# Optimization experiments

Measured on AMD Instinct MI355X. Metric: run time of the kernel, lower is better.

## Reference

```python
import jax, jax.numpy as jnp
import numpy as np

N = 1_000_000
DATA_DIM = 16
N_COND = 8            # conditions 1..8; condition 0 uses the base model (id 0)
N_BUCKETS = 8         # uniform time intervals per condition on [0,1)
N_MODELS = N_COND * N_BUCKETS + 1   # 65, matches num_models+1 in the torch ctor
HIDDEN = 6            # SimpleModel(data_dim, hidden=6, time_embed_dim=6)
IN_DIM = DATA_DIM + 1 # MLP input is cat([data, t], dim=1)


def setup_inputs() -> dict:
    key = jax.random.key(0)
    k_data, k_cond, k_t, k_w1, k_b1, k_w2, k_b2 = jax.random.split(key, 7)
    data = jax.random.normal(k_data, (N, DATA_DIM), dtype=jnp.float32)
    cond = jax.random.randint(k_cond, (N, 1), 0, N_COND + 1).astype(jnp.float32)  # 0..8
    t = jax.random.uniform(k_t, (N, 1), dtype=jnp.float32)                        # [0,1)
    x = jnp.concatenate([data, cond, t], axis=1)  # [N, DATA_DIM+2]
    s1 = 1.0 / np.sqrt(IN_DIM)
    s2 = 1.0 / np.sqrt(HIDDEN)
    W1 = jax.random.uniform(k_w1, (N_MODELS, IN_DIM, HIDDEN), jnp.float32, -s1, s1)
    b1 = jax.random.uniform(k_b1, (N_MODELS, HIDDEN), jnp.float32, -s1, s1)
    W2 = jax.random.uniform(k_w2, (N_MODELS, HIDDEN, DATA_DIM), jnp.float32, -s2, s2)
    b2 = jax.random.uniform(k_b2, (N_MODELS, DATA_DIM), jnp.float32, -s2, s2)
    return {"x": x, "W1": W1, "b1": b1, "W2": W2, "b2": b2}


def _route(cond_f, t):
    # Bucket routing: cond 0 -> model 0 on [0,1); cond c>=1 -> models 1 + (c-1)*8 + floor(t*8).
    # Equivalent to the torch per-(c, [t1,t2)) masked dispatch with uniform breakpoints.
    c = cond_f.astype(jnp.int32)
    bucket = jnp.clip(jnp.floor(t * N_BUCKETS).astype(jnp.int32), 0, N_BUCKETS - 1)
    return jnp.where(c == 0, 0, 1 + (c - 1) * N_BUCKETS + bucket)


def reference(x, W1, b1, W2, b2):
    data = x[:, :-2]
    cond = x[:, -2]
    t = x[:, -1]
    mid = _route(cond, t)                                   # [N] expert id per row
    xin = jnp.concatenate([data, t[:, None]], axis=1)       # [N, IN_DIM]
    # Fused gather-MLP: gather each row's tiny expert weights and apply the 2-layer MLP.
    h = jax.nn.relu(jnp.einsum('ni,nih->nh', xin, W1[mid]) + b1[mid])   # [N, HIDDEN]
    out = jnp.einsum('nh,nhd->nd', h, W2[mid]) + b2[mid]                # [N, DATA_DIM]
    return out
```

## Files before the change

kernel.cpp:

```cpp
#include <hip/hip_runtime.h>


#define NMODELS 65
#define WPM 220
#define NCHUNK 55
#define BLOCK 512

__global__ __launch_bounds__(BLOCK, 4) void mvf_kernel(
    const float* __restrict__ x,
    const float* __restrict__ W1,
    const float* __restrict__ b1,
    const float* __restrict__ W2,
    const float* __restrict__ b2,
    float* __restrict__ out,
    int npts)
{
    __shared__ float4 wlds[NCHUNK][NMODELS];
    const int tid = threadIdx.x;

    float* wf = (float*)wlds;
    for (int e = tid; e < NMODELS * WPM; e += BLOCK) {
        const int m = e / WPM, k = e % WPM;
        float v;
        if (k < 102)      v = W1[m * 102 + k];
        else if (k < 108) v = b1[m * 6 + (k - 102)];
        else if (k < 204) v = W2[m * 96 + (k - 108)];
        else              v = b2[m * 16 + (k - 204)];
        wf[(k >> 2) * (NMODELS * 4) + m * 4 + (k & 3)] = v;
    }
    __syncthreads();

    const int q = blockIdx.x * BLOCK + tid;
    const int p0 = 2 * q;
    if (p0 >= npts) return;

    float xf[36];
    {
        const float4* xr4 = (const float4*)(x + (long)p0 * 18);
        #pragma unroll
        for (int i = 0; i < 9; ++i) {
            float4 v = xr4[i];
            xf[4 * i + 0] = v.x;
            xf[4 * i + 1] = v.y;
            xf[4 * i + 2] = v.z;
            xf[4 * i + 3] = v.w;
        }
    }
    #define XF(pt, i) xf[(pt) * 18 + (i)]

    int mid[2];
    float tt[2];
    #pragma unroll
    for (int pt = 0; pt < 2; ++pt) {
        const float t = XF(pt, 17);
        const int c = (int)XF(pt, 16);
        int bucket = (int)floorf(t * 8.0f);
        bucket = bucket < 0 ? 0 : (bucket > 7 ? 7 : bucket);
        mid[pt] = (c == 0) ? 0 : 1 + (c - 1) * 8 + bucket;
        tt[pt] = t;
    }

    #define CH(cc, pt) wlds[cc][mid[pt]]

    float h[2][6];
    #pragma unroll
    for (int pt = 0; pt < 2; ++pt) {
        float4 c24 = CH(24, pt);
        float4 c25 = CH(25, pt);
        float4 c26 = CH(26, pt);
        const float t = tt[pt];
        h[pt][0] = fmaf(t, c24.x, c25.z);
        h[pt][1] = fmaf(t, c24.y, c25.w);
        h[pt][2] = fmaf(t, c24.z, c26.x);
        h[pt][3] = fmaf(t, c24.w, c26.y);
        h[pt][4] = fmaf(t, c25.x, c26.z);
        h[pt][5] = fmaf(t, c25.y, c26.w);
    }
    #pragma unroll
    for (int r = 0; r < 8; ++r) {
        #pragma unroll
        for (int pt = 0; pt < 2; ++pt) {
            float4 a = CH(3 * r + 0, pt);
            float4 b = CH(3 * r + 1, pt);
            float4 d = CH(3 * r + 2, pt);
            const float x0 = XF(pt, 2 * r), x1 = XF(pt, 2 * r + 1);
            h[pt][0] = fmaf(x0, a.x, h[pt][0]);
            h[pt][1] = fmaf(x0, a.y, h[pt][1]);
            h[pt][2] = fmaf(x0, a.z, h[pt][2]);
            h[pt][3] = fmaf(x0, a.w, h[pt][3]);
            h[pt][4] = fmaf(x0, b.x, h[pt][4]);
            h[pt][5] = fmaf(x0, b.y, h[pt][5]);
            h[pt][0] = fmaf(x1, b.z, h[pt][0]);
            h[pt][1] = fmaf(x1, b.w, h[pt][1]);
            h[pt][2] = fmaf(x1, d.x, h[pt][2]);
            h[pt][3] = fmaf(x1, d.y, h[pt][3]);
            h[pt][4] = fmaf(x1, d.z, h[pt][4]);
            h[pt][5] = fmaf(x1, d.w, h[pt][5]);
        }
    }
    #pragma unroll
    for (int pt = 0; pt < 2; ++pt)
        #pragma unroll
        for (int j = 0; j < 6; ++j)
            h[pt][j] = h[pt][j] > 0.0f ? h[pt][j] : 0.0f;

    #pragma unroll
    for (int half = 0; half < 2; ++half) {
        #pragma unroll
        for (int pt = 0; pt < 2; ++pt) {
            float o[8];
            {
                float4 ba = CH(51 + 2 * half, pt);
                float4 bb = CH(52 + 2 * half, pt);
                o[0] = ba.x; o[1] = ba.y; o[2] = ba.z; o[3] = ba.w;
                o[4] = bb.x; o[5] = bb.y; o[6] = bb.z; o[7] = bb.w;
            }
            #pragma unroll
            for (int j = 0; j < 6; ++j) {
                float4 A = CH(27 + 4 * j + 2 * half + 0, pt);
                float4 B = CH(27 + 4 * j + 2 * half + 1, pt);
                const float hj = h[pt][j];
                o[0] = fmaf(hj, A.x, o[0]);
                o[1] = fmaf(hj, A.y, o[1]);
                o[2] = fmaf(hj, A.z, o[2]);
                o[3] = fmaf(hj, A.w, o[3]);
                o[4] = fmaf(hj, B.x, o[4]);
                o[5] = fmaf(hj, B.y, o[5]);
                o[6] = fmaf(hj, B.z, o[6]);
                o[7] = fmaf(hj, B.w, o[7]);
            }
            float4* orow = (float4*)(out + (long)(p0 + pt) * 16 + half * 8);
            orow[0] = make_float4(o[0], o[1], o[2], o[3]);
            orow[1] = make_float4(o[4], o[5], o[6], o[7]);
        }
    }
    #undef CH
    #undef XF
}

extern "C" void kernel_launch(void* const* d_in, const int* in_sizes, int n_in,
                              void* d_out, int out_size, void* d_ws, size_t ws_size,
                              hipStream_t stream) {
    const float* x  = (const float*)d_in[0];
    const float* W1 = (const float*)d_in[1];
    const float* b1 = (const float*)d_in[2];
    const float* W2 = (const float*)d_in[3];
    const float* b2 = (const float*)d_in[4];
    float* out = (float*)d_out;

    const int npts = in_sizes[0] / 18;
    const int npairs = (npts + 1) / 2;
    const int grid = (npairs + BLOCK - 1) / BLOCK;
    mvf_kernel<<<grid, BLOCK, 0, stream>>>(x, W1, b1, W2, b2, out, npts);
}
```

Baseline: 48.90 us.

## Double block size, load routing fields first, and compute all outputs before storing

Raises the block size to 1024 so the per-block LDS weight staging is amortized over twice as many points. It loads the cond/t float4s first so routing can start while the remaining input loads are in flight. The second layer now keeps all 16 outputs of both points in registers and writes them with consecutive float4 stores at the end. This raises register pressure, which under launch_bounds(1024,4) may cause spills, and the larger block reduces how many blocks can be resident at once.

```diff
diff --git a/kernel.cpp b/kernel.cpp
--- a/kernel.cpp
+++ b/kernel.cpp
@@ -4,7 +4,7 @@
 #define NMODELS 65
 #define WPM 220
 #define NCHUNK 55
-#define BLOCK 512
+#define BLOCK 1024
 
 __global__ __launch_bounds__(BLOCK, 4) void mvf_kernel(
     const float* __restrict__ x,
@@ -34,32 +34,40 @@
     const int p0 = 2 * q;
     if (p0 >= npts) return;
 
+    const float4* xr4 = (const float4*)(x + (long)p0 * 18);
+
     float xf[36];
     {
-        const float4* xr4 = (const float4*)(x + (long)p0 * 18);
-        #pragma unroll
-        for (int i = 0; i < 9; ++i) {
-            float4 v = xr4[i];
-            xf[4 * i + 0] = v.x;
-            xf[4 * i + 1] = v.y;
-            xf[4 * i + 2] = v.z;
-            xf[4 * i + 3] = v.w;
-        }
+        float4 v4 = xr4[4];
+        float4 v8 = xr4[8];
+        xf[16] = v4.x; xf[17] = v4.y; xf[18] = v4.z; xf[19] = v4.w;
+        xf[32] = v8.x; xf[33] = v8.y; xf[34] = v8.z; xf[35] = v8.w;
     }
-    #define XF(pt, i) xf[(pt) * 18 + (i)]
-
     int mid[2];
     float tt[2];
     #pragma unroll
     for (int pt = 0; pt < 2; ++pt) {
-        const float t = XF(pt, 17);
-        const int c = (int)XF(pt, 16);
+        const float t = xf[pt * 18 + 17];
+        const int c = (int)xf[pt * 18 + 16];
         int bucket = (int)floorf(t * 8.0f);
         bucket = bucket < 0 ? 0 : (bucket > 7 ? 7 : bucket);
         mid[pt] = (c == 0) ? 0 : 1 + (c - 1) * 8 + bucket;
         tt[pt] = t;
     }
 
+    #pragma unroll
+    for (int i = 0; i < 4; ++i) {
+        float4 v = xr4[i];
+        xf[4 * i + 0] = v.x; xf[4 * i + 1] = v.y;
+        xf[4 * i + 2] = v.z; xf[4 * i + 3] = v.w;
+    }
+    #pragma unroll
+    for (int i = 5; i < 8; ++i) {
+        float4 v = xr4[i];
+        xf[4 * i + 0] = v.x; xf[4 * i + 1] = v.y;
+        xf[4 * i + 2] = v.z; xf[4 * i + 3] = v.w;
+    }
+    #define XF(pt, i) xf[(pt) * 18 + (i)]
     #define CH(cc, pt) wlds[cc][mid[pt]]
 
     float h[2][6];
@@ -104,38 +112,43 @@
         for (int j = 0; j < 6; ++j)
             h[pt][j] = h[pt][j] > 0.0f ? h[pt][j] : 0.0f;
 
+    float o[2][16];
     #pragma unroll
-    for (int half = 0; half < 2; ++half) {
+    for (int pt = 0; pt < 2; ++pt) {
+        #pragma unroll
+        for (int g = 0; g < 4; ++g) {
+            float4 v = CH(51 + g, pt);
+            o[pt][4 * g + 0] = v.x;
+            o[pt][4 * g + 1] = v.y;
+            o[pt][4 * g + 2] = v.z;
+            o[pt][4 * g + 3] = v.w;
+        }
+    }
+    #pragma unroll
+    for (int j = 0; j < 6; ++j) {
         #pragma unroll
         for (int pt = 0; pt < 2; ++pt) {
-            float o[8];
-            {
-                float4 ba = CH(51 + 2 * half, pt);
-                float4 bb = CH(52 + 2 * half, pt);
-                o[0] = ba.x; o[1] = ba.y; o[2] = ba.z; o[3] = ba.w;
-                o[4] = bb.x; o[5] = bb.y; o[6] = bb.z; o[7] = bb.w;
+            const float hj = h[pt][j];
+            #pragma unroll
+            for (int g = 0; g < 4; ++g) {
+                float4 v = CH(27 + 4 * j + g, pt);
+                o[pt][4 * g + 0] = fmaf(hj, v.x, o[pt][4 * g + 0]);
+                o[pt][4 * g + 1] = fmaf(hj, v.y, o[pt][4 * g + 1]);
+                o[pt][4 * g + 2] = fmaf(hj, v.z, o[pt][4 * g + 2]);
+                o[pt][4 * g + 3] = fmaf(hj, v.w, o[pt][4 * g + 3]);
             }
-            #pragma unroll
-            for (int j = 0; j < 6; ++j) {
-                float4 A = CH(27 + 4 * j + 2 * half + 0, pt);
-                float4 B = CH(27 + 4 * j + 2 * half + 1, pt);
-                const float hj = h[pt][j];
-                o[0] = fmaf(hj, A.x, o[0]);
-                o[1] = fmaf(hj, A.y, o[1]);
-                o[2] = fmaf(hj, A.z, o[2]);
-                o[3] = fmaf(hj, A.w, o[3]);
-                o[4] = fmaf(hj, B.x, o[4]);
-                o[5] = fmaf(hj, B.y, o[5]);
-                o[6] = fmaf(hj, B.z, o[6]);
-                o[7] = fmaf(hj, B.w, o[7]);
-            }
-            float4* orow = (float4*)(out + (long)(p0 + pt) * 16 + half * 8);
-            orow[0] = make_float4(o[0], o[1], o[2], o[3]);
-            orow[1] = make_float4(o[4], o[5], o[6], o[7]);
         }
     }
     #undef CH
     #undef XF
+
+    float4* orow = (float4*)(out + (long)p0 * 16);
+    #pragma unroll
+    for (int pt = 0; pt < 2; ++pt)
+        #pragma unroll
+        for (int g = 0; g < 4; ++g)
+            orow[4 * pt + g] = make_float4(o[pt][4 * g], o[pt][4 * g + 1],
+                                           o[pt][4 * g + 2], o[pt][4 * g + 3]);
 }
 
 extern "C" void kernel_launch(void* const* d_in, const int* in_sizes, int n_in,
```

New measurement: 46.22 us. 1.06x faster.
